# Kernel tuning notes

Measured on AMD Instinct MI355X. Metric: run time of the kernel, lower is better.

## Reference

```python
import jax, jax.numpy as jnp
import numpy as np

B, T, P, E = 4, 16, 256, 768
H, D = 12, 64          # num_heads, kq_size; H*D == E
DFF = 3072
SCALE = D ** (-0.5)
EPS = 1e-5


def _ln(x, g, b):
    m = jnp.mean(x, axis=-1, keepdims=True)
    v = jnp.mean((x - m) ** 2, axis=-1, keepdims=True)
    return (x - m) / jnp.sqrt(v + EPS) * g + b


def setup_inputs() -> dict:
    key = jax.random.key(0)
    ks = jax.random.split(key, 16)
    std = 0.02
    d = {"x": jax.random.normal(ks[0], (B, T, P, E), jnp.float32)}
    # spatial attention params (weights stored as (in, out))
    d["sq_w"] = jax.random.normal(ks[1], (E, H * D), jnp.float32) * std
    d["sk_w"] = jax.random.normal(ks[2], (E, H * D), jnp.float32) * std
    d["sv_w"] = jax.random.normal(ks[3], (E, H * D), jnp.float32) * std
    d["so_w"] = jax.random.normal(ks[4], (H * D, E), jnp.float32) * std
    d["sq_b"] = jnp.zeros((H * D,), jnp.float32)
    d["sk_b"] = jnp.zeros((H * D,), jnp.float32)
    d["sv_b"] = jnp.zeros((H * D,), jnp.float32)
    d["so_b"] = jnp.zeros((E,), jnp.float32)
    d["sg"] = jnp.ones((E,), jnp.float32)
    d["sb"] = jnp.zeros((E,), jnp.float32)
    # temporal attention params
    d["tq_w"] = jax.random.normal(ks[5], (E, H * D), jnp.float32) * std
    d["tk_w"] = jax.random.normal(ks[6], (E, H * D), jnp.float32) * std
    d["tv_w"] = jax.random.normal(ks[7], (E, H * D), jnp.float32) * std
    d["to_w"] = jax.random.normal(ks[8], (H * D, E), jnp.float32) * std
    d["tq_b"] = jnp.zeros((H * D,), jnp.float32)
    d["tk_b"] = jnp.zeros((H * D,), jnp.float32)
    d["tv_b"] = jnp.zeros((H * D,), jnp.float32)
    d["to_b"] = jnp.zeros((E,), jnp.float32)
    d["tg"] = jnp.ones((E,), jnp.float32)
    d["tb"] = jnp.zeros((E,), jnp.float32)
    # FFN + final layernorm
    d["w1"] = jax.random.normal(ks[9], (E, DFF), jnp.float32) * std
    d["b1"] = jnp.zeros((DFF,), jnp.float32)
    d["w2"] = jax.random.normal(ks[10], (DFF, E), jnp.float32) * std
    d["b2"] = jnp.zeros((E,), jnp.float32)
    d["g"] = jnp.ones((E,), jnp.float32)
    d["bb"] = jnp.zeros((E,), jnp.float32)
    return d


def reference(x, sq_w, sq_b, sk_w, sk_b, sv_w, sv_b, so_w, so_b, sg, sb,
              tq_w, tq_b, tk_w, tk_b, tv_w, tv_b, to_w, to_b, tg, tb,
              w1, b1, w2, b2, g, bb):
    b, t, p, e = x.shape

    # ---- Spatial layer: attention over patches P within each frame ----
    q = (x @ sq_w + sq_b).reshape(b, t, p, H, D)
    k = (x @ sk_w + sk_b).reshape(b, t, p, H, D)
    v = (x @ sv_w + sv_b).reshape(b, t, p, H, D)
    attn = jnp.einsum('btphd,btqhd->bthpq', q, k) * SCALE
    attn = jax.nn.softmax(attn, axis=-1)
    out = jnp.einsum('bthpq,btqhd->btphd', attn, v).reshape(b, t, p, H * D)
    out = out @ so_w + so_b
    x = _ln(x + out, sg, sb)

    # ---- Temporal layer: causal attention over frames T per patch ----
    q = (x @ tq_w + tq_b).reshape(b, t, p, H, D)
    k = (x @ tk_w + tk_b).reshape(b, t, p, H, D)
    v = (x @ tv_w + tv_b).reshape(b, t, p, H, D)
    attn = jnp.einsum('btphd,bsphd->bphts', q, k) * SCALE
    causal = jnp.where(jnp.arange(t)[:, None] >= jnp.arange(t)[None, :],
                       jnp.float32(0), -jnp.inf).astype(x.dtype)  # (T, T)
    attn = attn + causal
    attn = jax.nn.softmax(attn, axis=-1)
    out = jnp.einsum('bphts,bsphd->btphd', attn, v).reshape(b, t, p, H * D)
    out = out @ to_w + to_b
    x = _ln(x + out, tg, tb)

    # ---- Feed forward + final layernorm ----
    ff = jax.nn.gelu(x @ w1 + b1, approximate=False) @ w2 + b2
    x = _ln(x + ff, g, bb)
    return x
```

## Files before the change

kernel.cpp:

```cpp
#include <hip/hip_runtime.h>
#include <math.h>

constexpr int cB   = 4;
constexpr int cT   = 16;
constexpr int cP   = 256;
constexpr int cE   = 768;
constexpr int cH   = 12;
constexpr int cD   = 64;
constexpr int cDFF = 3072;
constexpr int NTOK = cB * cT * cP;
constexpr float cSCALE = 0.125f;
constexpr float cEPS = 1e-5f;

typedef __attribute__((ext_vector_type(8))) short short8;
typedef __attribute__((ext_vector_type(4))) float f32x4;
typedef __attribute__((ext_vector_type(8))) unsigned short u16x8;
typedef __attribute__((ext_vector_type(4))) unsigned short u16x4;

#define AS1 __attribute__((address_space(1)))
#define AS3 __attribute__((address_space(3)))

__device__ inline float b2f(unsigned short u) {
    union { unsigned int i; float f; } c; c.i = ((unsigned int)u) << 16; return c.f;
}
__device__ inline unsigned short f2b(float f) {
    union { float f; unsigned int i; } c; c.f = f;
    unsigned int i = c.i;
    unsigned int r = i + 0x7FFFu + ((i >> 16) & 1u);
    return (unsigned short)(r >> 16);
}

__device__ inline void gload16(const unsigned short* g, short* l) {
    __builtin_amdgcn_global_load_lds((AS1 const void*)g, (AS3 void*)l, 16, 0, 0);
}

template<int OUTB, int ACT, int SPLIT3>
__global__ __launch_bounds__(512, 2) void gemm256_kernel(
    const unsigned short* __restrict__ A,
    const unsigned short* __restrict__ BT,
    const float* __restrict__ bias0, const float* __restrict__ bias1,
    const float* __restrict__ bias2,
    void* __restrict__ C0, void* __restrict__ C1, void* __restrict__ C2,
    int M, int N, int K, int nbn)
{
    __shared__ short LDS[3 * 24576];

    const int tid = threadIdx.x;
    const int w = tid >> 6, l = tid & 63;
    const int l15 = l & 15, l16 = l >> 4;
    const int wm = w >> 1, wn = w & 1;
    const int srow = l >> 3;
    const int sslot = l & 7;

    const int nwg = gridDim.x;
    const int wg = (blockIdx.x & 7) * (nwg >> 3) + (blockIdx.x >> 3);
    const int bm = wg / nbn, bn = wg % nbn;
    const int m0 = bm * 256, n0 = bn * 128;

    const unsigned short* pA = A + (size_t)m0 * K;
    const unsigned short* pB = BT + (size_t)n0 * K;

    f32x4 acc[4][4];
    #pragma unroll
    for (int i = 0; i < 4; ++i)
        #pragma unroll
        for (int j = 0; j < 4; ++j)
            #pragma unroll
            for (int r = 0; r < 4; ++r) acc[i][j][r] = 0.f;

    const int nt = K >> 6;

    #define STAGE_A(t_, buf_)                                                   \
        {                                                                       \
            const unsigned short* src_ = pA + (t_) * 64;                        \
            short* dst_ = LDS + (buf_) * 24576;                                 \
            _Pragma("unroll")                                                   \
            for (int j_ = 0; j_ < 4; ++j_) {                                    \
                const int r_ = w * 32 + j_ * 8 + srow;                          \
                gload16(src_ + (size_t)r_ * K + ((sslot ^ (r_ & 7)) << 3),      \
                        dst_ + r_ * 64 + (sslot << 3));                         \
            }                                                                   \
        }
    #define STAGE_B(t_, buf_)                                                   \
        {                                                                       \
            const unsigned short* src_ = pB + (t_) * 64;                        \
            short* dst_ = LDS + (buf_) * 24576 + 16384;                         \
            _Pragma("unroll")                                                   \
            for (int j_ = 0; j_ < 2; ++j_) {                                    \
                const int r_ = w * 8 + j_ * 64 + srow;                          \
                gload16(src_ + (size_t)r_ * K + ((sslot ^ (r_ & 7)) << 3),      \
                        dst_ + r_ * 64 + (sslot << 3));                         \
            }                                                                   \
        }

    STAGE_A(0, 0); STAGE_B(0, 0);
    STAGE_A(1, 1); STAGE_B(1, 1);
    asm volatile("s_waitcnt vmcnt(6)" ::: "memory");
    __builtin_amdgcn_s_barrier();

    int buf = 0;
    for (int t = 0; t < nt; ++t) {
        const short* bA = LDS + buf * 24576;
        const short* bB = bA + 16384;

        short8 aF[4][2], bF[4][2];
        #pragma unroll
        for (int mm = 0; mm < 4; ++mm) {
            const int ra = wm * 64 + mm * 16 + l15;
            const char* pa = (const char*)bA + ra * 128;
            aF[mm][0] = *(const short8*)(pa + ((l16 * 16) ^ ((ra & 7) << 4)));
        }
        #pragma unroll
        for (int nf = 0; nf < 4; ++nf) {
            const int rb = wn * 64 + nf * 16 + l15;
            const char* pb = (const char*)bB + rb * 128;
            bF[nf][0] = *(const short8*)(pb + ((l16 * 16) ^ ((rb & 7) << 4)));
        }
        __builtin_amdgcn_sched_barrier(0);
        #pragma unroll
        for (int mm = 0; mm < 4; ++mm) {
            const int ra = wm * 64 + mm * 16 + l15;
            const char* pa = (const char*)bA + ra * 128;
            aF[mm][1] = *(const short8*)(pa + ((64 + l16 * 16) ^ ((ra & 7) << 4)));
        }
        #pragma unroll
        for (int nf = 0; nf < 4; ++nf) {
            const int rb = wn * 64 + nf * 16 + l15;
            const char* pb = (const char*)bB + rb * 128;
            bF[nf][1] = *(const short8*)(pb + ((64 + l16 * 16) ^ ((rb & 7) << 4)));
        }

        if (t + 2 < nt) {
            const int b2 = (buf == 0) ? 2 : buf - 1;
            STAGE_A(t + 2, b2); STAGE_B(t + 2, b2);
        }

        asm volatile("s_waitcnt lgkmcnt(8)" ::: "memory");
        __builtin_amdgcn_sched_barrier(0);
        __builtin_amdgcn_s_setprio(1);
        #pragma unroll
        for (int nf = 0; nf < 4; ++nf)
            #pragma unroll
            for (int mm = 0; mm < 4; ++mm)
                acc[mm][nf] = __builtin_amdgcn_mfma_f32_16x16x32_bf16(
                    aF[mm][0], bF[nf][0], acc[mm][nf], 0, 0, 0);
        __builtin_amdgcn_s_setprio(0);
        asm volatile("s_waitcnt lgkmcnt(0)" ::: "memory");
        __builtin_amdgcn_sched_barrier(0);
        __builtin_amdgcn_s_setprio(1);
        #pragma unroll
        for (int nf = 0; nf < 4; ++nf)
            #pragma unroll
            for (int mm = 0; mm < 4; ++mm)
                acc[mm][nf] = __builtin_amdgcn_mfma_f32_16x16x32_bf16(
                    aF[mm][1], bF[nf][1], acc[mm][nf], 0, 0, 0);
        __builtin_amdgcn_s_setprio(0);

        if (t + 1 < nt) {
            if (t + 2 < nt)
                asm volatile("s_waitcnt vmcnt(6)" ::: "memory");
            else
                asm volatile("s_waitcnt vmcnt(0)" ::: "memory");
            __builtin_amdgcn_s_barrier();
        }
        buf = (buf == 2) ? 0 : buf + 1;
    }
    #undef STAGE_A
    #undef STAGE_B

    #pragma unroll
    for (int mf = 0; mf < 4; ++mf) {
        #pragma unroll
        for (int nf = 0; nf < 4; ++nf) {
            const int ng = n0 + wn * 64 + nf * 16 + l15;
            int nl = ng;
            const float* bp = bias0;
            void* Cp = C0;
            int Nout = N;
            if (SPLIT3) {
                const int which = ng / 768;
                nl = ng - which * 768;
                bp = (which == 0) ? bias0 : (which == 1) ? bias1 : bias2;
                Cp = (which == 0) ? C0 : (which == 1) ? C1 : C2;
                Nout = 768;
            }
            const float bs = bp[nl];
            #pragma unroll
            for (int r = 0; r < 4; ++r) {
                const int row = m0 + wm * 64 + mf * 16 + l16 * 4 + r;
                float v = acc[mf][nf][r] + bs;
                if (ACT) v = 0.5f * v * (1.f + erff(v * 0.70710678118654752f));
                if (OUTB) ((unsigned short*)Cp)[(size_t)row * Nout + nl] = f2b(v);
                else      ((float*)Cp)[(size_t)row * Nout + nl] = v;
            }
        }
    }
}

__global__ __launch_bounds__(256) void transpose_cast_kernel(
    const float* __restrict__ W, unsigned short* __restrict__ WT,
    int K, int N)
{
    __shared__ float t[32][33];
    const int k0 = blockIdx.y * 32;
    const int n0 = blockIdx.x * 32;
    const int tx = threadIdx.x & 31;
    const int ty4 = (threadIdx.x >> 5) << 2;
    #pragma unroll
    for (int i = 0; i < 4; ++i)
        t[ty4 + i][tx] = W[(size_t)(k0 + ty4 + i) * N + n0 + tx];
    __syncthreads();
    #pragma unroll
    for (int i = 0; i < 4; ++i)
        WT[(size_t)(n0 + ty4 + i) * K + k0 + tx] = f2b(t[tx][ty4 + i]);
}

struct TP8 { const float* src[8]; unsigned short* dst[8]; };
__global__ __launch_bounds__(256) void transpose_cast8_kernel(TP8 p)
{
    __shared__ float t[32][33];
    const int z = blockIdx.z;
    const float* W = p.src[z];
    unsigned short* WT = p.dst[z];
    const int k0 = blockIdx.y * 32;
    const int n0 = blockIdx.x * 32;
    const int tx = threadIdx.x & 31;
    const int ty4 = (threadIdx.x >> 5) << 2;
    #pragma unroll
    for (int i = 0; i < 4; ++i)
        t[ty4 + i][tx] = W[(size_t)(k0 + ty4 + i) * cE + n0 + tx];
    __syncthreads();
    #pragma unroll
    for (int i = 0; i < 4; ++i)
        WT[(size_t)(n0 + ty4 + i) * cE + k0 + tx] = f2b(t[tx][ty4 + i]);
}

__global__ __launch_bounds__(256) void cast_bf16_kernel(
    const float* __restrict__ in, unsigned short* __restrict__ out, int n4)
{
    for (int i = blockIdx.x * blockDim.x + threadIdx.x; i < n4;
         i += gridDim.x * blockDim.x) {
        float4 v = ((const float4*)in)[i];
        u16x4 o;
        o[0] = f2b(v.x); o[1] = f2b(v.y); o[2] = f2b(v.z); o[3] = f2b(v.w);
        *(u16x4*)(out + (size_t)i * 4) = o;
    }
}

__global__ __launch_bounds__(256) void residual_ln_kernel(
    const float* __restrict__ X, const float* __restrict__ R,
    const float* __restrict__ gamma, const float* __restrict__ beta,
    float* __restrict__ out, unsigned short* __restrict__ outb)
{
    const int row = blockIdx.x;
    const size_t off = (size_t)row * cE;
    const int tid = threadIdx.x;

    float v[3];
    float s = 0.f, ss = 0.f;
    #pragma unroll
    for (int i = 0; i < 3; ++i) {
        const int e = tid + i * 256;
        const float t = X[off + e] + R[off + e];
        v[i] = t; s += t; ss += t * t;
    }
    #pragma unroll
    for (int o = 32; o > 0; o >>= 1) {
        s  += __shfl_down(s, o);
        ss += __shfl_down(ss, o);
    }
    __shared__ float rs[4], rss[4];
    const int wid = tid >> 6;
    if ((tid & 63) == 0) { rs[wid] = s; rss[wid] = ss; }
    __syncthreads();
    s  = rs[0] + rs[1] + rs[2] + rs[3];
    ss = rss[0] + rss[1] + rss[2] + rss[3];

    const float mean = s * (1.f / cE);
    const float var  = ss * (1.f / cE) - mean * mean;
    const float inv  = rsqrtf(var + cEPS);
    #pragma unroll
    for (int i = 0; i < 3; ++i) {
        const int e = tid + i * 256;
        const float r = (v[i] - mean) * inv * gamma[e] + beta[e];
        out[off + e] = r;
        if (outb) outb[off + e] = f2b(r);
    }
}

__global__ __launch_bounds__(256) void spatial_attn_mfma_kernel(
    const unsigned short* __restrict__ Q, const unsigned short* __restrict__ K,
    const unsigned short* __restrict__ V, unsigned short* __restrict__ O)
{
    __shared__ short Ks[64 * 64];
    __shared__ short Vt[64 * 64];
    __shared__ short Ps[4][64 * 64];

    const int bid = blockIdx.x;
    const int h  = bid % cH;
    const int bt = bid / cH;
    const size_t base = (size_t)bt * cP * cE + h * cD;

    const int tid = threadIdx.x;
    const int w = tid >> 6, l = tid & 63;
    const int l15 = l & 15, l16 = l >> 4;

    short8 qf[4][2];
    #pragma unroll
    for (int mf = 0; mf < 4; ++mf)
        #pragma unroll
        for (int kf = 0; kf < 2; ++kf)
            qf[mf][kf] = *(const short8*)(
                Q + base + (size_t)(w * 64 + mf * 16 + l15) * cE + kf * 32 + l16 * 8);

    f32x4 o[4][4];
    float mrun[4][4], lrun[4][4];
    #pragma unroll
    for (int mf = 0; mf < 4; ++mf)
        #pragma unroll
        for (int j = 0; j < 4; ++j) {
            #pragma unroll
            for (int r = 0; r < 4; ++r) o[mf][j][r] = 0.f;
            mrun[mf][j] = -INFINITY; lrun[mf][j] = 0.f;
        }

    const int krow = w * 8 + (l >> 3);
    const int kc16 = l & 7;
    const int vj  = tid & 31;
    const int vd0 = (tid >> 5) * 8;

    for (int c0 = 0; c0 < cP; c0 += 64) {
        __syncthreads();
        #pragma unroll
        for (int p = 0; p < 2; ++p) {
            const int row = p * 32 + krow;
            gload16(K + base + (size_t)(c0 + row) * cE + ((kc16 ^ (row & 7)) << 3),
                    Ks + row * 64 + kc16 * 8);
        }
        #pragma unroll
        for (int p = 0; p < 2; ++p) {
            const int j = p * 32 + vj;
            short8 vv = *(const short8*)(V + base + (size_t)(c0 + j) * cE + vd0);
            char* vb = (char*)Vt;
            #pragma unroll
            for (int e = 0; e < 8; ++e) {
                const int row = vd0 + e;
                *(short*)(vb + row * 128 + ((2 * j) ^ ((row & 7) << 4))) = vv[e];
            }
        }
        __syncthreads();

        f32x4 s[4][4];
        #pragma unroll
        for (int mf = 0; mf < 4; ++mf)
            #pragma unroll
            for (int nf = 0; nf < 4; ++nf)
                #pragma unroll
                for (int r = 0; r < 4; ++r) s[mf][nf][r] = 0.f;

        #pragma unroll
        for (int nf = 0; nf < 4; ++nf) {
            const int row = nf * 16 + l15;
            const char* kb = (const char*)Ks + row * 128;
            const int sw = (row & 7) << 4;
            short8 k0 = *(const short8*)(kb + ((l16 * 16) ^ sw));
            short8 k1 = *(const short8*)(kb + ((64 + l16 * 16) ^ sw));
            #pragma unroll
            for (int mf = 0; mf < 4; ++mf) {
                s[mf][nf] = __builtin_amdgcn_mfma_f32_16x16x32_bf16(qf[mf][0], k0, s[mf][nf], 0, 0, 0);
                s[mf][nf] = __builtin_amdgcn_mfma_f32_16x16x32_bf16(qf[mf][1], k1, s[mf][nf], 0, 0, 0);
            }
        }

        #pragma unroll
        for (int mf = 0; mf < 4; ++mf)
            #pragma unroll
            for (int nf = 0; nf < 4; ++nf)
                #pragma unroll
                for (int r = 0; r < 4; ++r) s[mf][nf][r] *= cSCALE;

        #pragma unroll
        for (int mf = 0; mf < 4; ++mf) {
            #pragma unroll
            for (int r = 0; r < 4; ++r) {
                float rv = fmaxf(fmaxf(s[mf][0][r], s[mf][1][r]),
                                 fmaxf(s[mf][2][r], s[mf][3][r]));
                rv = fmaxf(rv, __shfl_xor(rv, 1));
                rv = fmaxf(rv, __shfl_xor(rv, 2));
                rv = fmaxf(rv, __shfl_xor(rv, 4));
                rv = fmaxf(rv, __shfl_xor(rv, 8));
                const float mn = fmaxf(mrun[mf][r], rv);
                const float al = __expf(mrun[mf][r] - mn);
                mrun[mf][r] = mn;
                float ps = 0.f;
                #pragma unroll
                for (int nf = 0; nf < 4; ++nf) {
                    const float pe = __expf(s[mf][nf][r] - mn);
                    s[mf][nf][r] = pe;
                    ps += pe;
                }
                ps += __shfl_xor(ps, 1);
                ps += __shfl_xor(ps, 2);
                ps += __shfl_xor(ps, 4);
                ps += __shfl_xor(ps, 8);
                lrun[mf][r] = lrun[mf][r] * al + ps;
                #pragma unroll
                for (int df = 0; df < 4; ++df) o[mf][df][r] *= al;
            }
        }

        char* pw = (char*)&Ps[w][0];
        #pragma unroll
        for (int mf = 0; mf < 4; ++mf)
            #pragma unroll
            for (int nf = 0; nf < 4; ++nf)
                #pragma unroll
                for (int r = 0; r < 4; ++r) {
                    const int row = mf * 16 + l16 * 4 + r;
                    *(short*)(pw + row * 128 + (((nf * 16 + l15) * 2) ^ ((row & 7) << 4))) =
                        (short)f2b(s[mf][nf][r]);
                }

        short8 pa[4][2];
        #pragma unroll
        for (int mf = 0; mf < 4; ++mf) {
            const int prow = mf * 16 + l15;
            const char* pb = (const char*)&Ps[w][0] + prow * 128;
            const int sw = (prow & 7) << 4;
            pa[mf][0] = *(const short8*)(pb + ((l16 * 16) ^ sw));
            pa[mf][1] = *(const short8*)(pb + ((64 + l16 * 16) ^ sw));
        }
        #pragma unroll
        for (int df = 0; df < 4; ++df) {
            const int vrow = df * 16 + l15;
            const char* vbb = (const char*)Vt + vrow * 128;
            const int sw = (vrow & 7) << 4;
            short8 v0 = *(const short8*)(vbb + ((l16 * 16) ^ sw));
            short8 v1 = *(const short8*)(vbb + ((64 + l16 * 16) ^ sw));
            #pragma unroll
            for (int mf = 0; mf < 4; ++mf) {
                o[mf][df] = __builtin_amdgcn_mfma_f32_16x16x32_bf16(pa[mf][0], v0, o[mf][df], 0, 0, 0);
                o[mf][df] = __builtin_amdgcn_mfma_f32_16x16x32_bf16(pa[mf][1], v1, o[mf][df], 0, 0, 0);
            }
        }
    }

    #pragma unroll
    for (int mf = 0; mf < 4; ++mf)
        #pragma unroll
        for (int r = 0; r < 4; ++r) {
            const float inv = 1.f / lrun[mf][r];
            const size_t rowoff = base + (size_t)(w * 64 + mf * 16 + l16 * 4 + r) * cE;
            #pragma unroll
            for (int df = 0; df < 4; ++df)
                O[rowoff + df * 16 + l15] = f2b(o[mf][df][r] * inv);
        }
}

__global__ __launch_bounds__(128) void temporal_attn_kernel(
    const unsigned short* __restrict__ Q, const unsigned short* __restrict__ Kb,
    const unsigned short* __restrict__ V, unsigned short* __restrict__ O)
{
    const int bid = blockIdx.x;
    const int hg  = bid & 1;
    const int bp  = bid >> 1;
    const int p   = bp % cP;
    const int b   = bp / cP;

    __shared__ float Ks[cT][6][cD + 1];
    __shared__ float Vs[cT][6][cD + 1];

    const size_t framestride = (size_t)cP * cE;
    const size_t base0 = ((size_t)(b * cT) * cP + p) * cE + hg * 384;

    for (int li = threadIdx.x; li < cT * 384; li += 128) {
        const int s = li / 384;
        const int r = li % 384;
        const size_t src = base0 + (size_t)s * framestride + r;
        Ks[s][r / 64][r & 63] = b2f(Kb[src]);
        Vs[s][r / 64][r & 63] = b2f(V[src]);
    }
    __syncthreads();
    if (threadIdx.x >= 96) return;

    const int hh = threadIdx.x >> 4;
    const int t  = threadIdx.x & 15;
    const size_t qoff = ((size_t)(b * cT + t) * cP + p) * cE + hg * 384 + hh * cD;

    float q[cD];
    #pragma unroll
    for (int d = 0; d < cD; d += 8) {
        short8 f = *(const short8*)(Q + qoff + d);
        #pragma unroll
        for (int j = 0; j < 8; ++j) q[d + j] = b2f((unsigned short)f[j]);
    }

    float sc[cT];
    float mx = -INFINITY;
    #pragma unroll
    for (int s = 0; s < cT; ++s) {
        float acc = 0.f;
        #pragma unroll
        for (int d = 0; d < cD; ++d) acc = fmaf(q[d], Ks[s][hh][d], acc);
        sc[s] = (s <= t) ? acc * cSCALE : -INFINITY;
        mx = fmaxf(mx, sc[s]);
    }
    float l = 0.f;
    #pragma unroll
    for (int s = 0; s < cT; ++s) {
        const float e_ = __expf(sc[s] - mx);
        sc[s] = e_;
        l += e_;
    }
    float o[cD];
    #pragma unroll
    for (int d = 0; d < cD; ++d) o[d] = 0.f;
    #pragma unroll
    for (int s = 0; s < cT; ++s) {
        const float pj = sc[s];
        #pragma unroll
        for (int d = 0; d < cD; ++d) o[d] = fmaf(pj, Vs[s][hh][d], o[d]);
    }
    const float invl = 1.f / l;
    unsigned short* op = O + qoff;
    #pragma unroll
    for (int d = 0; d < cD; d += 8) {
        u16x8 f;
        #pragma unroll
        for (int j = 0; j < 8; ++j) f[j] = f2b(o[d + j] * invl);
        *(u16x8*)(op + d) = f;
    }
}

extern "C" void kernel_launch(void* const* d_in, const int* in_sizes, int n_in,
                              void* d_out, int out_size, void* d_ws, size_t ws_size,
                              hipStream_t stream)
{
    const float* x    = (const float*)d_in[0];
    const float* sq_w = (const float*)d_in[1];
    const float* sk_w = (const float*)d_in[2];
    const float* sv_w = (const float*)d_in[3];
    const float* so_w = (const float*)d_in[4];
    const float* sq_b = (const float*)d_in[5];
    const float* sk_b = (const float*)d_in[6];
    const float* sv_b = (const float*)d_in[7];
    const float* so_b = (const float*)d_in[8];
    const float* sg   = (const float*)d_in[9];
    const float* sb   = (const float*)d_in[10];
    const float* tq_w = (const float*)d_in[11];
    const float* tk_w = (const float*)d_in[12];
    const float* tv_w = (const float*)d_in[13];
    const float* to_w = (const float*)d_in[14];
    const float* tq_b = (const float*)d_in[15];
    const float* tk_b = (const float*)d_in[16];
    const float* tv_b = (const float*)d_in[17];
    const float* to_b = (const float*)d_in[18];
    const float* tg   = (const float*)d_in[19];
    const float* tb   = (const float*)d_in[20];
    const float* w1   = (const float*)d_in[21];
    const float* b1   = (const float*)d_in[22];
    const float* w2   = (const float*)d_in[23];
    const float* b2   = (const float*)d_in[24];
    const float* g    = (const float*)d_in[25];
    const float* bb   = (const float*)d_in[26];

    const size_t NE = (size_t)NTOK * cE;
    const size_t EE = (size_t)cE * cE;

    float* W0 = (float*)d_ws;
    float* Wp = W0 + NE;
    unsigned short* Xb = (unsigned short*)(Wp + NE);
    unsigned short* Qb = Xb + NE;
    unsigned short* Kbuf = Qb + NE;
    unsigned short* Vb = Kbuf + NE;
    unsigned short* Ob = Vb + NE;
    unsigned short* Hb = Qb;
    unsigned short* WT = Ob + NE;
    unsigned short* sqT = WT;
    unsigned short* skT = sqT + EE;
    unsigned short* svT = skT + EE;
    unsigned short* soT = svT + EE;
    unsigned short* tqT = soT + EE;
    unsigned short* tkT = tqT + EE;
    unsigned short* tvT = tkT + EE;
    unsigned short* toT = tvT + EE;
    unsigned short* w1T = toT + EE;
    unsigned short* w2T = w1T + (size_t)cDFF * cE;

    const dim3 blk(256);
    const dim3 blk512(512);
    const dim3 gLN(NTOK);
    const dim3 gQKV(1152);
    const dim3 gOUT(384);
    const dim3 gFF1(1536);

    cast_bf16_kernel<<<dim3(2048), blk, 0, stream>>>(x, Xb, (int)(NE / 4));
    {
        TP8 p;
        p.src[0] = sq_w; p.dst[0] = sqT;
        p.src[1] = sk_w; p.dst[1] = skT;
        p.src[2] = sv_w; p.dst[2] = svT;
        p.src[3] = so_w; p.dst[3] = soT;
        p.src[4] = tq_w; p.dst[4] = tqT;
        p.src[5] = tk_w; p.dst[5] = tkT;
        p.src[6] = tv_w; p.dst[6] = tvT;
        p.src[7] = to_w; p.dst[7] = toT;
        transpose_cast8_kernel<<<dim3(cE / 32, cE / 32, 8), blk, 0, stream>>>(p);
    }
    transpose_cast_kernel<<<dim3(cDFF / 32, cE / 32), blk, 0, stream>>>(w1, w1T, cE, cDFF);
    transpose_cast_kernel<<<dim3(cE / 32, cDFF / 32), blk, 0, stream>>>(w2, w2T, cDFF, cE);

    gemm256_kernel<1,0,1><<<gQKV, blk512, 0, stream>>>(
        Xb, sqT, sq_b, sk_b, sv_b, Qb, Kbuf, Vb, NTOK, 2304, cE, 18);
    spatial_attn_mfma_kernel<<<dim3(cB * cT * cH), blk, 0, stream>>>(Qb, Kbuf, Vb, Ob);
    gemm256_kernel<0,0,0><<<gOUT, blk512, 0, stream>>>(
        Ob, soT, so_b, nullptr, nullptr, Wp, nullptr, nullptr, NTOK, cE, cE, 6);
    residual_ln_kernel<<<gLN, blk, 0, stream>>>(x, Wp, sg, sb, W0, Xb);

    gemm256_kernel<1,0,1><<<gQKV, blk512, 0, stream>>>(
        Xb, tqT, tq_b, tk_b, tv_b, Qb, Kbuf, Vb, NTOK, 2304, cE, 18);
    temporal_attn_kernel<<<dim3(cB * cP * 2), dim3(128), 0, stream>>>(Qb, Kbuf, Vb, Ob);
    gemm256_kernel<0,0,0><<<gOUT, blk512, 0, stream>>>(
        Ob, toT, to_b, nullptr, nullptr, Wp, nullptr, nullptr, NTOK, cE, cE, 6);
    residual_ln_kernel<<<gLN, blk, 0, stream>>>(W0, Wp, tg, tb, W0, Xb);

    gemm256_kernel<1,1,0><<<gFF1, blk512, 0, stream>>>(
        Xb, w1T, b1, nullptr, nullptr, Hb, nullptr, nullptr, NTOK, cDFF, cE, 24);
    gemm256_kernel<0,0,0><<<gOUT, blk512, 0, stream>>>(
        Hb, w2T, b2, nullptr, nullptr, Wp, nullptr, nullptr, NTOK, cE, cDFF, 6);
    residual_ln_kernel<<<gLN, blk, 0, stream>>>(W0, Wp, g, bb, (float*)d_out, nullptr);
}
```

Before: 710.8 us.

## Split GEMM K-step into two phases interleaving LDS reads, staging, and MFMAs

Restructures the inner GEMM loop into two half-tiles over M. Each phase reads its A fragments (B fragments once), issues half of the next-next tile's global-to-LDS staging (A in the first phase, B in the second), then runs that phase's MFMAs. Extra workgroup barriers are placed around each phase so the waves stay in step. The aim is to spread global loads and LDS traffic across the MFMA work instead of issuing them in one burst, at the cost of additional s_barrier synchronisation per K-step.

```diff
diff --git a/kernel.cpp b/kernel.cpp
--- a/kernel.cpp
+++ b/kernel.cpp
@@ -102,59 +102,67 @@
     for (int t = 0; t < nt; ++t) {
         const short* bA = LDS + buf * 24576;
         const short* bB = bA + 16384;
+        const int sbuf = (buf < 1) ? buf + 2 : buf - 1;
 
         short8 aF[4][2], bF[4][2];
-        #pragma unroll
-        for (int mm = 0; mm < 4; ++mm) {
-            const int ra = wm * 64 + mm * 16 + l15;
-            const char* pa = (const char*)bA + ra * 128;
-            aF[mm][0] = *(const short8*)(pa + ((l16 * 16) ^ ((ra & 7) << 4)));
-        }
         #pragma unroll
         for (int nf = 0; nf < 4; ++nf) {
             const int rb = wn * 64 + nf * 16 + l15;
             const char* pb = (const char*)bB + rb * 128;
-            bF[nf][0] = *(const short8*)(pb + ((l16 * 16) ^ ((rb & 7) << 4)));
-        }
-        __builtin_amdgcn_sched_barrier(0);
-        #pragma unroll
-        for (int mm = 0; mm < 4; ++mm) {
+            const int sw = (rb & 7) << 4;
+            bF[nf][0] = *(const short8*)(pb + ((l16 * 16) ^ sw));
+            bF[nf][1] = *(const short8*)(pb + ((64 + l16 * 16) ^ sw));
+        }
+        #pragma unroll
+        for (int mm = 0; mm < 2; ++mm) {
             const int ra = wm * 64 + mm * 16 + l15;
             const char* pa = (const char*)bA + ra * 128;
-            aF[mm][1] = *(const short8*)(pa + ((64 + l16 * 16) ^ ((ra & 7) << 4)));
-        }
-        #pragma unroll
-        for (int nf = 0; nf < 4; ++nf) {
-            const int rb = wn * 64 + nf * 16 + l15;
-            const char* pb = (const char*)bB + rb * 128;
-            bF[nf][1] = *(const short8*)(pb + ((64 + l16 * 16) ^ ((rb & 7) << 4)));
-        }
-
-        if (t + 2 < nt) {
-            const int b2 = (buf == 0) ? 2 : buf - 1;
-            STAGE_A(t + 2, b2); STAGE_B(t + 2, b2);
-        }
-
-        asm volatile("s_waitcnt lgkmcnt(8)" ::: "memory");
-        __builtin_amdgcn_sched_barrier(0);
-        __builtin_amdgcn_s_setprio(1);
-        #pragma unroll
-        for (int nf = 0; nf < 4; ++nf)
-            #pragma unroll
-            for (int mm = 0; mm < 4; ++mm)
-                acc[mm][nf] = __builtin_amdgcn_mfma_f32_16x16x32_bf16(
-                    aF[mm][0], bF[nf][0], acc[mm][nf], 0, 0, 0);
-        __builtin_amdgcn_s_setprio(0);
+            const int sw = (ra & 7) << 4;
+            aF[mm][0] = *(const short8*)(pa + ((l16 * 16) ^ sw));
+            aF[mm][1] = *(const short8*)(pa + ((64 + l16 * 16) ^ sw));
+        }
+        if (t + 2 < nt) { STAGE_A(t + 2, sbuf); }
+
+        __builtin_amdgcn_s_barrier();
         asm volatile("s_waitcnt lgkmcnt(0)" ::: "memory");
         __builtin_amdgcn_sched_barrier(0);
         __builtin_amdgcn_s_setprio(1);
         #pragma unroll
-        for (int nf = 0; nf < 4; ++nf)
-            #pragma unroll
-            for (int mm = 0; mm < 4; ++mm)
-                acc[mm][nf] = __builtin_amdgcn_mfma_f32_16x16x32_bf16(
-                    aF[mm][1], bF[nf][1], acc[mm][nf], 0, 0, 0);
+        for (int kk = 0; kk < 2; ++kk)
+            #pragma unroll
+            for (int nf = 0; nf < 4; ++nf)
+                #pragma unroll
+                for (int mm = 0; mm < 2; ++mm)
+                    acc[mm][nf] = __builtin_amdgcn_mfma_f32_16x16x32_bf16(
+                        aF[mm][kk], bF[nf][kk], acc[mm][nf], 0, 0, 0);
         __builtin_amdgcn_s_setprio(0);
+        __builtin_amdgcn_sched_barrier(0);
+        __builtin_amdgcn_s_barrier();
+
+        #pragma unroll
+        for (int mm = 2; mm < 4; ++mm) {
+            const int ra = wm * 64 + mm * 16 + l15;
+            const char* pa = (const char*)bA + ra * 128;
+            const int sw = (ra & 7) << 4;
+            aF[mm][0] = *(const short8*)(pa + ((l16 * 16) ^ sw));
+            aF[mm][1] = *(const short8*)(pa + ((64 + l16 * 16) ^ sw));
+        }
+        if (t + 2 < nt) { STAGE_B(t + 2, sbuf); }
+
+        __builtin_amdgcn_s_barrier();
+        asm volatile("s_waitcnt lgkmcnt(0)" ::: "memory");
+        __builtin_amdgcn_sched_barrier(0);
+        __builtin_amdgcn_s_setprio(1);
+        #pragma unroll
+        for (int kk = 0; kk < 2; ++kk)
+            #pragma unroll
+            for (int nf = 0; nf < 4; ++nf)
+                #pragma unroll
+                for (int mm = 2; mm < 4; ++mm)
+                    acc[mm][nf] = __builtin_amdgcn_mfma_f32_16x16x32_bf16(
+                        aF[mm][kk], bF[nf][kk], acc[mm][nf], 0, 0, 0);
+        __builtin_amdgcn_s_setprio(0);
+        __builtin_amdgcn_sched_barrier(0);
 
         if (t + 1 < nt) {
             if (t + 2 < nt)
```

After: 753.5 us. 6.0% more time.
